# Optimization experiments

Hardware: AMD Instinct MI355X
Metric: run time of the kernel (lower is better)

The kernel has to match this reference:

```python
import jax, jax.numpy as jnp
import numpy as np
import math

B, T, C, H = 2, 2048, 1024, 16

def setup_inputs() -> dict:
    key = jax.random.key(0)
    ks = jax.random.split(key, 5)
    s = 0.02
    return {
        "x": jax.random.normal(ks[0], (B, T, C), dtype=jnp.float32),
        "W_attn": jax.random.normal(ks[1], (C, 3 * C), dtype=jnp.float32) * s,
        "b_attn": jnp.zeros((3 * C,), dtype=jnp.float32),
        "W_proj": jax.random.normal(ks[2], (C, C), dtype=jnp.float32) * s,
        "b_proj": jnp.zeros((C,), dtype=jnp.float32),
    }

def reference(x, W_attn, b_attn, W_proj, b_proj):
    Bx, Tx, Cx = x.shape
    hd = Cx // H  # head dim = 64
    qkv = x @ W_attn + b_attn                      # [B,T,3C]
    q, k, v = jnp.split(qkv, 3, axis=-1)
    # [B,H,T,hd]
    q = q.reshape(Bx, Tx, H, hd).transpose(0, 2, 1, 3)
    k = k.reshape(Bx, Tx, H, hd).transpose(0, 2, 1, 3)
    v = v.reshape(Bx, Tx, H, hd).transpose(0, 2, 1, 3)
    scale = 1.0 / math.sqrt(hd)
    att = jnp.einsum('bhqd,bhkd->bhqk', q, k) * scale   # [B,H,T,T]
    causal = jnp.tril(jnp.ones((Tx, Tx), dtype=bool))
    att = jnp.where(causal[None, None, :, :], att, -jnp.inf)
    att = jax.nn.softmax(att, axis=-1)
    y = jnp.einsum('bhqk,bhkd->bhqd', att, v)           # [B,H,T,hd]
    y = y.transpose(0, 2, 1, 3).reshape(Bx, Tx, Cx)
    return y @ W_proj + b_proj
```

## Files before the change

### kernel.cpp

```cpp
#include <hip/hip_runtime.h>

typedef __attribute__((ext_vector_type(8))) __bf16 bf16x8;
typedef __attribute__((ext_vector_type(4))) float f32x4;

#define T_SEQ 2048
#define NH 16
#define HD 64
#define CDIM 1024
#define NQK 2048
#define NQKV 3072
#define MTOT 4096

#define SWZ(r, c) ((((r) * 8) + ((c) ^ ((r) & 7))) * 8)

__device__ __forceinline__ void async_load16(const void* g, void* l) {
    __builtin_amdgcn_global_load_lds(
        (const __attribute__((address_space(1))) void*)g,
        (__attribute__((address_space(3))) void*)l, 16, 0, 0);
}

__global__ __launch_bounds__(256) void cvt_bf16_kernel(const float* __restrict__ in,
                                                       __bf16* __restrict__ out, int n) {
    int i = (blockIdx.x * 256 + threadIdx.x) * 8;
    if (i + 8 <= n) {
        float4 f0 = *(const float4*)(in + i);
        float4 f1 = *(const float4*)(in + i + 4);
        bf16x8 o;
        o[0] = (__bf16)f0.x; o[1] = (__bf16)f0.y; o[2] = (__bf16)f0.z; o[3] = (__bf16)f0.w;
        o[4] = (__bf16)f1.x; o[5] = (__bf16)f1.y; o[6] = (__bf16)f1.z; o[7] = (__bf16)f1.w;
        *(bf16x8*)(out + i) = o;
    }
}

__global__ __launch_bounds__(256) void transpose_bf16_kernel(const float* __restrict__ in,
                                                             __bf16* __restrict__ out,
                                                             int R, int C) {
    __shared__ float tile[32][33];
    int c0 = blockIdx.x * 32, r0 = blockIdx.y * 32;
    int tx = threadIdx.x, ty = threadIdx.y;
#pragma unroll
    for (int i = 0; i < 4; i++)
        tile[ty + i * 8][tx] = in[(size_t)(r0 + ty + i * 8) * C + c0 + tx];
    __syncthreads();
#pragma unroll
    for (int i = 0; i < 4; i++)
        out[(size_t)(c0 + ty + i * 8) * R + r0 + tx] = (__bf16)tile[tx][ty + i * 8];
}

template <int WNW>
__global__ __launch_bounds__(256) void gemm_bt_kernel(
    const __bf16* __restrict__ A, const __bf16* __restrict__ Bt,
    const float* __restrict__ bias, int M, int N, int K, int mode,
    __bf16* __restrict__ qkb, __bf16* __restrict__ vtb, float* __restrict__ outf)
{
    constexpr int MI = (WNW == 2) ? 4 : 2;
    constexpr int BROWS = WNW * 64;
    __shared__ __bf16 As[128 * 64];
    __shared__ __bf16 Bs[BROWS * 64];

    int tid = threadIdx.x;
    int lane = tid & 63, wid = tid >> 6;
    int quad = lane >> 4, r16 = lane & 15;
    int wm = (WNW == 2) ? (wid >> 1) * 64 : wid * 32;
    int wn = (WNW == 2) ? (wid & 1) * 64 : 0;
    int bm = blockIdx.y * 128, bn = blockIdx.x * (WNW * 64);

    f32x4 acc[MI][4] = {};

    int lrow = lane >> 3;
    int lcolsw = (((lane & 7) ^ (lrow & 7)) * 8);
    const __bf16* Ag = A + (size_t)(bm + wid * 32 + lrow) * K + lcolsw;
    const __bf16* Bg = Bt + (size_t)(bn + wid * (BROWS / 4) + lrow) * K + lcolsw;
    char* lA = (char*)As + wid * 4096;
    char* lB = (char*)Bs + wid * (BROWS / 4) * 128;

    for (int kt = 0; kt < K; kt += 64) {
        __syncthreads();
#pragma unroll
        for (int i = 0; i < 4; i++)
            async_load16(Ag + kt + (size_t)i * 8 * K, lA + i * 1024);
#pragma unroll
        for (int i = 0; i < BROWS / 32; i++)
            async_load16(Bg + kt + (size_t)i * 8 * K, lB + i * 1024);
        __syncthreads();
#pragma unroll
        for (int ks = 0; ks < 2; ks++) {
            bf16x8 af[MI], bfr[4];
#pragma unroll
            for (int i = 0; i < MI; i++)
                af[i] = *(const bf16x8*)&As[SWZ(wm + i * 16 + r16, ks * 4 + quad)];
#pragma unroll
            for (int i = 0; i < 4; i++)
                bfr[i] = *(const bf16x8*)&Bs[SWZ(wn + i * 16 + r16, ks * 4 + quad)];
#pragma unroll
            for (int mi = 0; mi < MI; mi++)
#pragma unroll
                for (int ni = 0; ni < 4; ni++)
                    acc[mi][ni] = __builtin_amdgcn_mfma_f32_16x16x32_bf16(
                        af[mi], bfr[ni], acc[mi][ni], 0, 0, 0);
        }
    }

    const float SC2 = 0.125f * 1.44269504088896f;
#pragma unroll
    for (int mi = 0; mi < MI; mi++) {
#pragma unroll
        for (int ni = 0; ni < 4; ni++) {
            int col = bn + wn + ni * 16 + r16;
            float bv = bias[col];
            int row0 = bm + wm + mi * 16 + quad * 4;
            if (mode == 1) {
#pragma unroll
                for (int rg = 0; rg < 4; rg++)
                    outf[(size_t)(row0 + rg) * N + col] = acc[mi][ni][rg] + bv;
            } else if (col < 1024) {
#pragma unroll
                for (int rg = 0; rg < 4; rg++)
                    qkb[(size_t)(row0 + rg) * NQK + col] = (__bf16)((acc[mi][ni][rg] + bv) * SC2);
            } else if (col < 2048) {
#pragma unroll
                for (int rg = 0; rg < 4; rg++)
                    qkb[(size_t)(row0 + rg) * NQK + col] = (__bf16)(acc[mi][ni][rg] + bv);
            } else {
                int dcol = col - 2048;
                int b = row0 >> 11, t0 = row0 & 2047;
                union { __bf16 h[4]; uint2 u; } pk;
#pragma unroll
                for (int rg = 0; rg < 4; rg++) pk.h[rg] = (__bf16)(acc[mi][ni][rg] + bv);
                *(uint2*)&vtb[((size_t)b * 1024 + dcol) * T_SEQ + t0] = pk.u;
            }
        }
    }
}

__global__ __launch_bounds__(256) void attn_kernel(
    const __bf16* __restrict__ qkb, const __bf16* __restrict__ vtb,
    __bf16* __restrict__ y1)
{
    __shared__ __bf16 Ks[64 * 64];
    __shared__ __bf16 Vs[64 * 64];
    __shared__ __bf16 Ps[4][16][72];

    int tid = threadIdx.x;
    int lane = tid & 63, w = tid >> 6;
    int quad = lane >> 4, r16 = lane & 15;
    int bh = blockIdx.y;
    int b = bh >> 4, h = bh & 15;
    int qb = ((int)gridDim.x - 1 - (int)blockIdx.x) * 64;

    const __bf16* Qh = qkb + (size_t)b * T_SEQ * NQK + h * HD;
    const __bf16* Kh = Qh + CDIM;
    const __bf16* Vh = vtb + ((size_t)b * 1024 + h * HD) * T_SEQ;

    const float NEG_INF = -__builtin_inff();

    bf16x8 qf[2];
#pragma unroll
    for (int ks = 0; ks < 2; ks++)
        qf[ks] = *(const bf16x8*)(Qh + (size_t)(qb + w * 16 + r16) * NQK + ks * 32 + quad * 8);

    f32x4 o[4] = {};
    float m_i = NEG_INF, l_i = 0.f;

    int lrow = lane >> 3;
    int lcolsw = (((lane & 7) ^ (lrow & 7)) * 8);
    char* lK = (char*)Ks + w * 2048;
    char* lV = (char*)Vs + w * 2048;
    int qrow = qb + w * 16 + r16;
    int g0 = qb + w * 16;

    int nkt = qb / 64 + 1;
    for (int kt = 0; kt < nkt; kt++) {
        int kb = kt * 64;
        __syncthreads();
        const __bf16* kg = Kh + (size_t)(kb + w * 16 + lrow) * NQK + lcolsw;
        const __bf16* vg = Vh + (size_t)(w * 16 + lrow) * T_SEQ + kb + lcolsw;
        async_load16(kg, lK);
        async_load16(kg + (size_t)8 * NQK, lK + 1024);
        async_load16(vg, lV);
        async_load16(vg + (size_t)8 * T_SEQ, lV + 1024);
        __syncthreads();

        f32x4 s[4] = {};
#pragma unroll
        for (int ks = 0; ks < 2; ks++) {
            bf16x8 kf[4];
#pragma unroll
            for (int ni = 0; ni < 4; ni++)
                kf[ni] = *(const bf16x8*)&Ks[SWZ(ni * 16 + r16, ks * 4 + quad)];
#pragma unroll
            for (int ni = 0; ni < 4; ni++)
                s[ni] = __builtin_amdgcn_mfma_f32_16x16x32_bf16(kf[ni], qf[ks], s[ni], 0, 0, 0);
        }
        if (kb + 63 > g0) {
#pragma unroll
            for (int ni = 0; ni < 4; ni++)
#pragma unroll
                for (int rg = 0; rg < 4; rg++)
                    if (kb + ni * 16 + quad * 4 + rg > qrow) s[ni][rg] = NEG_INF;
        }
        float mx = NEG_INF;
#pragma unroll
        for (int ni = 0; ni < 4; ni++)
#pragma unroll
            for (int rg = 0; rg < 4; rg++) mx = fmaxf(mx, s[ni][rg]);
        mx = fmaxf(mx, __shfl_xor(mx, 16, 64));
        mx = fmaxf(mx, __shfl_xor(mx, 32, 64));
        float mnew = fmaxf(m_i, mx);
        float alpha = exp2f(m_i - mnew);
        float rs = 0.f;
#pragma unroll
        for (int ni = 0; ni < 4; ni++)
#pragma unroll
            for (int rg = 0; rg < 4; rg++) {
                float p = exp2f(s[ni][rg] - mnew);
                s[ni][rg] = p;
                rs += p;
            }
        rs += __shfl_xor(rs, 16, 64);
        rs += __shfl_xor(rs, 32, 64);
        l_i = l_i * alpha + rs;
        m_i = mnew;
#pragma unroll
        for (int nd = 0; nd < 4; nd++)
#pragma unroll
            for (int rg = 0; rg < 4; rg++) o[nd][rg] *= alpha;
#pragma unroll
        for (int ni = 0; ni < 4; ni++) {
            union { __bf16 h[4]; uint2 u; } pk;
#pragma unroll
            for (int rg = 0; rg < 4; rg++) pk.h[rg] = (__bf16)s[ni][rg];
            *(uint2*)&Ps[w][r16][ni * 16 + quad * 4] = pk.u;
        }
#pragma unroll
        for (int ks = 0; ks < 2; ks++) {
            bf16x8 vf[4];
#pragma unroll
            for (int nd = 0; nd < 4; nd++)
                vf[nd] = *(const bf16x8*)&Vs[SWZ(nd * 16 + r16, ks * 4 + quad)];
            bf16x8 pb = *(const bf16x8*)&Ps[w][r16][ks * 32 + quad * 8];
#pragma unroll
            for (int nd = 0; nd < 4; nd++)
                o[nd] = __builtin_amdgcn_mfma_f32_16x16x32_bf16(vf[nd], pb, o[nd], 0, 0, 0);
        }
    }

    float inv = 1.f / l_i;
    int t = qb + w * 16 + r16;
#pragma unroll
    for (int nd = 0; nd < 4; nd++) {
        union { __bf16 h[4]; uint2 u; } pk;
#pragma unroll
        for (int rg = 0; rg < 4; rg++) pk.h[rg] = (__bf16)(o[nd][rg] * inv);
        *(uint2*)&y1[(size_t)(b * T_SEQ + t) * CDIM + h * HD + nd * 16 + quad * 4] = pk.u;
    }
}

extern "C" void kernel_launch(void* const* d_in, const int* in_sizes, int n_in,
                              void* d_out, int out_size, void* d_ws, size_t ws_size,
                              hipStream_t stream) {
    const float* x = (const float*)d_in[0];
    const float* W_attn = (const float*)d_in[1];
    const float* b_attn = (const float*)d_in[2];
    const float* W_proj = (const float*)d_in[3];
    const float* b_proj = (const float*)d_in[4];
    float* out = (float*)d_out;

    char* p = (char*)d_ws;
    __bf16* xb = (__bf16*)p;   p += (size_t)MTOT * CDIM * 2;
    __bf16* WaT = (__bf16*)p;  p += (size_t)3 * CDIM * CDIM * 2;
    __bf16* WpT = (__bf16*)p;  p += (size_t)CDIM * CDIM * 2;
    __bf16* qkb = (__bf16*)p;  p += (size_t)MTOT * NQK * 2;
    __bf16* vtb = (__bf16*)p;  p += (size_t)2 * 1024 * T_SEQ * 2;
    __bf16* y1 = xb;

    cvt_bf16_kernel<<<2048, 256, 0, stream>>>(x, xb, MTOT * CDIM);
    transpose_bf16_kernel<<<dim3(96, 32), dim3(32, 8), 0, stream>>>(W_attn, WaT, CDIM, 3 * CDIM);
    transpose_bf16_kernel<<<dim3(32, 32), dim3(32, 8), 0, stream>>>(W_proj, WpT, CDIM, CDIM);
    gemm_bt_kernel<2><<<dim3(24, 32), 256, 0, stream>>>(xb, WaT, b_attn, MTOT, NQKV, CDIM, 0,
                                                        qkb, vtb, nullptr);
    attn_kernel<<<dim3(32, 32), 256, 0, stream>>>(qkb, vtb, y1);
    gemm_bt_kernel<1><<<dim3(16, 32), 256, 0, stream>>>(y1, WpT, b_proj, MTOT, CDIM, CDIM, 1,
                                                        nullptr, nullptr, out);
}
```

Before: 219.7 us.

## Pair complementary causal query tiles per attention block and merge transpose launches

Each attention block now processes query tile qt and its mirror 31-qt. This balances causal work across blocks and reuses each loaded K/V tile for both query tiles, halving the grid size. The two weight transpose kernels are merged into one launch to cut launch overhead. The pairing raises register use (two accumulator sets) and leaves fewer blocks in flight.

```diff
diff --git a/kernel.cpp b/kernel.cpp
--- a/kernel.cpp
+++ b/kernel.cpp
@@ -32,11 +32,14 @@
     }
 }
 
-__global__ __launch_bounds__(256) void transpose_bf16_kernel(const float* __restrict__ in,
-                                                             __bf16* __restrict__ out,
-                                                             int R, int C) {
+__global__ __launch_bounds__(256) void transpose2_kernel(
+    const float* __restrict__ Wa, const float* __restrict__ Wp,
+    __bf16* __restrict__ WaT, __bf16* __restrict__ WpT) {
     __shared__ float tile[32][33];
-    int c0 = blockIdx.x * 32, r0 = blockIdx.y * 32;
+    const float* in; __bf16* out; int C, bx = blockIdx.x;
+    if (bx < 96) { in = Wa; out = WaT; C = 3072; }
+    else         { in = Wp; out = WpT; C = 1024; bx -= 96; }
+    int c0 = bx * 32, r0 = blockIdx.y * 32;
     int tx = threadIdx.x, ty = threadIdx.y;
 #pragma unroll
     for (int i = 0; i < 4; i++)
@@ -44,7 +47,7 @@
     __syncthreads();
 #pragma unroll
     for (int i = 0; i < 4; i++)
-        out[(size_t)(c0 + ty + i * 8) * R + r0 + tx] = (__bf16)tile[tx][ty + i * 8];
+        out[(size_t)(c0 + ty + i * 8) * 1024 + r0 + tx] = (__bf16)tile[tx][ty + i * 8];
 }
 
 template <int WNW>
@@ -146,41 +149,32 @@
     int quad = lane >> 4, r16 = lane & 15;
     int bh = blockIdx.y;
     int b = bh >> 4, h = bh & 15;
-    int qb = ((int)gridDim.x - 1 - (int)blockIdx.x) * 64;
+    int qtA = blockIdx.x, qtB = 31 - qtA;
+    int qbA = qtA * 64, qbB = qtB * 64;
 
     const __bf16* Qh = qkb + (size_t)b * T_SEQ * NQK + h * HD;
     const __bf16* Kh = Qh + CDIM;
     const __bf16* Vh = vtb + ((size_t)b * 1024 + h * HD) * T_SEQ;
 
     const float NEG_INF = -__builtin_inff();
-
-    bf16x8 qf[2];
-#pragma unroll
-    for (int ks = 0; ks < 2; ks++)
-        qf[ks] = *(const bf16x8*)(Qh + (size_t)(qb + w * 16 + r16) * NQK + ks * 32 + quad * 8);
-
-    f32x4 o[4] = {};
-    float m_i = NEG_INF, l_i = 0.f;
-
     int lrow = lane >> 3;
     int lcolsw = (((lane & 7) ^ (lrow & 7)) * 8);
     char* lK = (char*)Ks + w * 2048;
     char* lV = (char*)Vs + w * 2048;
-    int qrow = qb + w * 16 + r16;
-    int g0 = qb + w * 16;
-
-    int nkt = qb / 64 + 1;
-    for (int kt = 0; kt < nkt; kt++) {
-        int kb = kt * 64;
-        __syncthreads();
-        const __bf16* kg = Kh + (size_t)(kb + w * 16 + lrow) * NQK + lcolsw;
-        const __bf16* vg = Vh + (size_t)(w * 16 + lrow) * T_SEQ + kb + lcolsw;
-        async_load16(kg, lK);
-        async_load16(kg + (size_t)8 * NQK, lK + 1024);
-        async_load16(vg, lV);
-        async_load16(vg + (size_t)8 * T_SEQ, lV + 1024);
-        __syncthreads();
-
+
+    bf16x8 qfA[2], qfB[2];
+#pragma unroll
+    for (int ks = 0; ks < 2; ks++) {
+        qfA[ks] = *(const bf16x8*)(Qh + (size_t)(qbA + w * 16 + r16) * NQK + ks * 32 + quad * 8);
+        qfB[ks] = *(const bf16x8*)(Qh + (size_t)(qbB + w * 16 + r16) * NQK + ks * 32 + quad * 8);
+    }
+    f32x4 oA[4] = {}, oB[4] = {};
+    float mA = NEG_INF, lA_ = 0.f, mB = NEG_INF, lB_ = 0.f;
+    int g0A = qbA + w * 16, g0B = qbB + w * 16;
+    int qrowA = g0A + r16, qrowB = g0B + r16;
+
+    auto tile_compute = [&](int kb, const bf16x8 (&qf)[2], f32x4 (&o)[4],
+                            float& m_i, float& l_i, int g0, int qrow) {
         f32x4 s[4] = {};
 #pragma unroll
         for (int ks = 0; ks < 2; ks++) {
@@ -243,16 +237,37 @@
             for (int nd = 0; nd < 4; nd++)
                 o[nd] = __builtin_amdgcn_mfma_f32_16x16x32_bf16(vf[nd], pb, o[nd], 0, 0, 0);
         }
-    }
-
-    float inv = 1.f / l_i;
-    int t = qb + w * 16 + r16;
-#pragma unroll
-    for (int nd = 0; nd < 4; nd++) {
-        union { __bf16 h[4]; uint2 u; } pk;
-#pragma unroll
-        for (int rg = 0; rg < 4; rg++) pk.h[rg] = (__bf16)(o[nd][rg] * inv);
-        *(uint2*)&y1[(size_t)(b * T_SEQ + t) * CDIM + h * HD + nd * 16 + quad * 4] = pk.u;
+    };
+
+    int nktA = qtA + 1, nktB = qtB + 1;
+    for (int kt = 0; kt < nktB; kt++) {
+        int kb = kt * 64;
+        __syncthreads();
+        const __bf16* kg = Kh + (size_t)(kb + w * 16 + lrow) * NQK + lcolsw;
+        const __bf16* vg = Vh + (size_t)(w * 16 + lrow) * T_SEQ + kb + lcolsw;
+        async_load16(kg, lK);
+        async_load16(kg + (size_t)8 * NQK, lK + 1024);
+        async_load16(vg, lV);
+        async_load16(vg + (size_t)8 * T_SEQ, lV + 1024);
+        __syncthreads();
+
+        tile_compute(kb, qfB, oB, mB, lB_, g0B, qrowB);
+        if (kt < nktA)
+            tile_compute(kb, qfA, oA, mA, lA_, g0A, qrowA);
+    }
+
+#pragma unroll
+    for (int which = 0; which < 2; which++) {
+        f32x4* o = which ? oB : oA;
+        float inv = 1.f / (which ? lB_ : lA_);
+        int t = (which ? qbB : qbA) + w * 16 + r16;
+#pragma unroll
+        for (int nd = 0; nd < 4; nd++) {
+            union { __bf16 h[4]; uint2 u; } pk;
+#pragma unroll
+            for (int rg = 0; rg < 4; rg++) pk.h[rg] = (__bf16)(o[nd][rg] * inv);
+            *(uint2*)&y1[(size_t)(b * T_SEQ + t) * CDIM + h * HD + nd * 16 + quad * 4] = pk.u;
+        }
     }
 }
 
@@ -275,11 +290,10 @@
     __bf16* y1 = xb;
 
     cvt_bf16_kernel<<<2048, 256, 0, stream>>>(x, xb, MTOT * CDIM);
-    transpose_bf16_kernel<<<dim3(96, 32), dim3(32, 8), 0, stream>>>(W_attn, WaT, CDIM, 3 * CDIM);
-    transpose_bf16_kernel<<<dim3(32, 32), dim3(32, 8), 0, stream>>>(W_proj, WpT, CDIM, CDIM);
+    transpose2_kernel<<<dim3(128, 32), dim3(32, 8), 0, stream>>>(W_attn, W_proj, WaT, WpT);
     gemm_bt_kernel<2><<<dim3(24, 32), 256, 0, stream>>>(xb, WaT, b_attn, MTOT, NQKV, CDIM, 0,
                                                         qkb, vtb, nullptr);
-    attn_kernel<<<dim3(32, 32), 256, 0, stream>>>(qkb, vtb, y1);
+    attn_kernel<<<dim3(16, 32), 256, 0, stream>>>(qkb, vtb, y1);
     gemm_bt_kernel<1><<<dim3(16, 32), 256, 0, stream>>>(y1, WpT, b_proj, MTOT, CDIM, CDIM, 1,
                                                         nullptr, nullptr, out);
 }
```

Result: faster. 199.5 us (-9.2%).
